# Kernel optimization log

Measured on AMD Instinct MI355X. Metric: run time of the kernel, lower is better.

Reference implementation:

```python
import jax, jax.numpy as jnp
import numpy as np

BINS = 10
LOSS_WEIGHT = 1.0
B = 8388608  # batch size
C = 2        # class num (hardcoded in the torch module's one-hot scatter)


def setup_inputs() -> dict:
    key = jax.random.key(0)
    k1, k2, k3 = jax.random.split(key, 3)
    pred = jax.random.normal(k1, (B, C), dtype=jnp.float32)
    target = jax.random.randint(k2, (B,), 0, 2, dtype=jnp.int64)
    # label_weight: 1 if valid, 0 if ignored (random 0/1 mask as float)
    label_weight = jax.random.randint(k3, (B, C), 0, 2).astype(jnp.float32)
    return {"pred": pred, "target": target, "label_weight": label_weight}


def reference(pred, target, label_weight):
    # one-hot target: torch scatter_(1, target, 1) over 2 classes
    t = jax.nn.one_hot(target, C, dtype=jnp.float32)  # [B, 2]
    # gradient norm g = |softmax(pred).detach() - target_onehot|
    g = jnp.abs(jax.lax.stop_gradient(jax.nn.softmax(pred, axis=1)) - t)  # [B, 2]
    valid = label_weight > 0
    valid_f = valid.astype(jnp.float32)
    total = jnp.maximum(valid_f.sum(), 1.0)
    # bin index: edges are i/bins with last edge nudged by 1e-6; uniform bins so
    # floor(g*bins) clipped to bins-1 reproduces the loop's (>= low) & (<= high)
    # assignment (ties on interior edges resolve to the upper bin, matching the
    # later-iteration overwrite in the torch loop).
    bin_ids = jnp.minimum((g * BINS).astype(jnp.int32), BINS - 1)  # [B, 2]
    # per-bin valid counts (histogram)
    counts = jnp.zeros((BINS,), jnp.float32).at[bin_ids].add(valid_f)
    n = jnp.maximum((counts > 0).sum().astype(jnp.float32), 1.0)
    # GHM weights: total / num_in_bin / n for valid entries, 0 otherwise
    w = jnp.where(valid, total / jnp.maximum(counts[bin_ids], 1.0) / n, 0.0)
    w = jax.lax.stop_gradient(w)
    # weighted BCE-with-logits, reduction='sum'
    bce = jnp.maximum(pred, 0.0) - pred * t + jnp.log1p(jnp.exp(-jnp.abs(pred)))
    loss = (w * bce).sum() / total
    return loss * LOSS_WEIGHT
```

## Files before the change

### kernel.cpp

```cpp
#include <hip/hip_runtime.h>

#define BINS 10
#define TPB  256
#define NBLK 2048
#define NCOPY 16

__device__ __forceinline__ unsigned long long ghm_pack(float p0, float p1, int t,
                                                       float w0, float w1, int* bin)
{
    bool tz = (t == 0);
    float x0 = tz ? -p0 : p0;
    float x1 = tz ?  p1 : -p1;
    float e0 = __expf(x0);
    float e1 = __expf(x1);
    float m  = e0 * e1;
    float g  = __fdividef(m, 1.0f + m);
    *bin = min((int)(g * 10.0f), BINS - 1);

    bool v0 = (w0 > 0.0f);
    bool v1 = (w1 > 0.0f);
    float a = v0 ? (1.0f + e0) : 1.0f;
    float b = v1 ? (1.0f + e1) : 1.0f;
    float wsum = __logf(a * b);
    unsigned long long cnt = (unsigned long long)((int)v0 + (int)v1);
    return (cnt << 48) | (unsigned long long)(unsigned int)(wsum * 1048576.0f + 0.5f);
}

__device__ __forceinline__ void ghm_2rows(float4 p, int2 t, float4 w,
                                          unsigned long long* hrow)
{
    int b0, b1;
    unsigned long long c0 = ghm_pack(p.x, p.y, t.x, w.x, w.y, &b0);
    unsigned long long c1 = ghm_pack(p.z, p.w, t.y, w.z, w.w, &b1);
    if (b0 == b1) {
        unsigned long long cs = c0 + c1;
        if (cs) atomicAdd(&hrow[b0], cs);
    } else {
        if (c0) atomicAdd(&hrow[b0], c0);
        if (c1) atomicAdd(&hrow[b1], c1);
    }
}

__global__ __launch_bounds__(TPB) void ghm_stage1(
    const float* __restrict__ pred, const int* __restrict__ target,
    const float* __restrict__ lw, unsigned long long* __restrict__ partial, int B)
{
    __shared__ unsigned long long h[NCOPY][BINS];
    for (int k = threadIdx.x; k < NCOPY * BINS; k += TPB)
        ((unsigned long long*)h)[k] = 0ULL;
    __syncthreads();

    unsigned long long* hrow = h[threadIdx.x >> 4];

    const float4* p4 = (const float4*)pred;
    const float4* w4 = (const float4*)lw;
    const int2*   t2 = (const int2*)target;
    const int npairs = B >> 1;
    const int stride = (int)gridDim.x * TPB;
    int i = blockIdx.x * TPB + threadIdx.x;

    for (; i + 3 * stride < npairs; i += 4 * stride) {
        float4 pa = p4[i];
        float4 pb = p4[i + stride];
        float4 pc = p4[i + 2 * stride];
        float4 pd = p4[i + 3 * stride];
        float4 wa = w4[i];
        float4 wb = w4[i + stride];
        float4 wc = w4[i + 2 * stride];
        float4 wd = w4[i + 3 * stride];
        int2   ta = t2[i];
        int2   tb = t2[i + stride];
        int2   tc = t2[i + 2 * stride];
        int2   td = t2[i + 3 * stride];
        ghm_2rows(pa, ta, wa, hrow);
        ghm_2rows(pb, tb, wb, hrow);
        ghm_2rows(pc, tc, wc, hrow);
        ghm_2rows(pd, td, wd, hrow);
    }
    for (; i < npairs; i += stride)
        ghm_2rows(p4[i], t2[i], w4[i], hrow);

    if ((B & 1) && blockIdx.x == 0 && threadIdx.x == 0) {
        int r = B - 1;
        int bb;
        unsigned long long cc = ghm_pack(pred[2 * r], pred[2 * r + 1], target[r],
                                         lw[2 * r], lw[2 * r + 1], &bb);
        if (cc) atomicAdd(&h[0][bb], cc);
    }
    __syncthreads();

    if (threadIdx.x < BINS) {
        unsigned long long v = 0;
#pragma unroll
        for (int c = 0; c < NCOPY; ++c) v += h[c][threadIdx.x];
        partial[blockIdx.x * BINS + threadIdx.x] = v;
    }
}

__global__ __launch_bounds__(TPB) void ghm_stage2(
    const unsigned long long* __restrict__ partial, float* __restrict__ out, int nb)
{
    double dsum[BINS], dcnt[BINS];
#pragma unroll
    for (int b = 0; b < BINS; ++b) { dsum[b] = 0.0; dcnt[b] = 0.0; }

    for (int i = threadIdx.x; i < nb; i += TPB) {
#pragma unroll
        for (int b = 0; b < BINS; ++b) {
            unsigned long long p = partial[i * BINS + b];
            dcnt[b] += (double)(p >> 48);
            dsum[b] += (double)(p & ((1ULL << 48) - 1)) * (1.0 / 1048576.0);
        }
    }

#pragma unroll
    for (int b = 0; b < BINS; ++b) {
        for (int off = 32; off > 0; off >>= 1) {
            dsum[b] += __shfl_down(dsum[b], off);
            dcnt[b] += __shfl_down(dcnt[b], off);
        }
    }

    __shared__ double ss[4][BINS];
    __shared__ double sc[4][BINS];
    const int wid  = threadIdx.x >> 6;
    const int lane = threadIdx.x & 63;
    if (lane == 0) {
#pragma unroll
        for (int b = 0; b < BINS; ++b) { ss[wid][b] = dsum[b]; sc[wid][b] = dcnt[b]; }
    }
    __syncthreads();

    if (threadIdx.x == 0) {
        double loss = 0.0;
        int n = 0;
        for (int b = 0; b < BINS; ++b) {
            double S = ss[0][b] + ss[1][b] + ss[2][b] + ss[3][b];
            double C = sc[0][b] + sc[1][b] + sc[2][b] + sc[3][b];
            if (C > 0.0) { ++n; loss += S / C; }
        }
        if (n == 0) n = 1;
        out[0] = (float)(loss / (double)n);
    }
}

extern "C" void kernel_launch(void* const* d_in, const int* in_sizes, int n_in,
                              void* d_out, int out_size, void* d_ws, size_t ws_size,
                              hipStream_t stream)
{
    const float* pred   = (const float*)d_in[0];
    const int*   target = (const int*)d_in[1];
    const float* lw     = (const float*)d_in[2];
    const int B = in_sizes[1];

    int nb = NBLK;
    size_t need = (size_t)nb * BINS * sizeof(unsigned long long);
    if (ws_size < need) nb = (int)(ws_size / (BINS * sizeof(unsigned long long)));

    unsigned long long* partial = (unsigned long long*)d_ws;

    ghm_stage1<<<nb, TPB, 0, stream>>>(pred, target, lw, partial, B);
    ghm_stage2<<<1, TPB, 0, stream>>>(partial, (float*)d_out, nb);
}
```

Baseline: 41.06 us.

## Issue all eight loads up front and transpose partials for a wider stage two

When the pair count is exactly eight grid strides, each thread issues all 24 vector loads before any computation, so more memory requests are in flight than the old four-way unrolled loop allowed. Per-block partial histograms are now stored bin-major, so stage two can read each bin with coalesced accesses across 1024 threads instead of 256. The fast path only applies when the input size matches the fixed grid exactly, and holding all loads in registers raises register pressure.

```diff
diff --git a/kernel.cpp b/kernel.cpp
--- a/kernel.cpp
+++ b/kernel.cpp
@@ -3,6 +3,7 @@
 #define BINS 10
 #define TPB  256
 #define NBLK 2048
+#define TPB2 1024
 #define NCOPY 16
 
 __device__ __forceinline__ unsigned long long ghm_pack(float p0, float p1, int t,
@@ -43,7 +44,7 @@
 
 __global__ __launch_bounds__(TPB) void ghm_stage1(
     const float* __restrict__ pred, const int* __restrict__ target,
-    const float* __restrict__ lw, unsigned long long* __restrict__ partial, int B)
+    const float* __restrict__ lw, unsigned long long* __restrict__ partialT, int B)
 {
     __shared__ unsigned long long h[NCOPY][BINS];
     for (int k = threadIdx.x; k < NCOPY * BINS; k += TPB)
@@ -57,35 +58,51 @@
     const int2*   t2 = (const int2*)target;
     const int npairs = B >> 1;
     const int stride = (int)gridDim.x * TPB;
-    int i = blockIdx.x * TPB + threadIdx.x;
+    const int i0 = blockIdx.x * TPB + threadIdx.x;
 
-    for (; i + 3 * stride < npairs; i += 4 * stride) {
-        float4 pa = p4[i];
-        float4 pb = p4[i + stride];
-        float4 pc = p4[i + 2 * stride];
-        float4 pd = p4[i + 3 * stride];
-        float4 wa = w4[i];
-        float4 wb = w4[i + stride];
-        float4 wc = w4[i + 2 * stride];
-        float4 wd = w4[i + 3 * stride];
-        int2   ta = t2[i];
-        int2   tb = t2[i + stride];
-        int2   tc = t2[i + 2 * stride];
-        int2   td = t2[i + 3 * stride];
-        ghm_2rows(pa, ta, wa, hrow);
-        ghm_2rows(pb, tb, wb, hrow);
-        ghm_2rows(pc, tc, wc, hrow);
-        ghm_2rows(pd, td, wd, hrow);
-    }
-    for (; i < npairs; i += stride)
-        ghm_2rows(p4[i], t2[i], w4[i], hrow);
-
-    if ((B & 1) && blockIdx.x == 0 && threadIdx.x == 0) {
-        int r = B - 1;
-        int bb;
-        unsigned long long cc = ghm_pack(pred[2 * r], pred[2 * r + 1], target[r],
-                                         lw[2 * r], lw[2 * r + 1], &bb);
-        if (cc) atomicAdd(&h[0][bb], cc);
+    if (npairs == 8 * stride) {
+        float4 P0 = p4[i0];
+        float4 P1 = p4[i0 + stride];
+        float4 P2 = p4[i0 + 2 * stride];
+        float4 P3 = p4[i0 + 3 * stride];
+        float4 P4 = p4[i0 + 4 * stride];
+        float4 P5 = p4[i0 + 5 * stride];
+        float4 P6 = p4[i0 + 6 * stride];
+        float4 P7 = p4[i0 + 7 * stride];
+        float4 W0 = w4[i0];
+        float4 W1 = w4[i0 + stride];
+        float4 W2 = w4[i0 + 2 * stride];
+        float4 W3 = w4[i0 + 3 * stride];
+        float4 W4 = w4[i0 + 4 * stride];
+        float4 W5 = w4[i0 + 5 * stride];
+        float4 W6 = w4[i0 + 6 * stride];
+        float4 W7 = w4[i0 + 7 * stride];
+        int2 T0 = t2[i0];
+        int2 T1 = t2[i0 + stride];
+        int2 T2 = t2[i0 + 2 * stride];
+        int2 T3 = t2[i0 + 3 * stride];
+        int2 T4 = t2[i0 + 4 * stride];
+        int2 T5 = t2[i0 + 5 * stride];
+        int2 T6 = t2[i0 + 6 * stride];
+        int2 T7 = t2[i0 + 7 * stride];
+        ghm_2rows(P0, T0, W0, hrow);
+        ghm_2rows(P1, T1, W1, hrow);
+        ghm_2rows(P2, T2, W2, hrow);
+        ghm_2rows(P3, T3, W3, hrow);
+        ghm_2rows(P4, T4, W4, hrow);
+        ghm_2rows(P5, T5, W5, hrow);
+        ghm_2rows(P6, T6, W6, hrow);
+        ghm_2rows(P7, T7, W7, hrow);
+    } else {
+        for (int i = i0; i < npairs; i += stride)
+            ghm_2rows(p4[i], t2[i], w4[i], hrow);
+        if ((B & 1) && blockIdx.x == 0 && threadIdx.x == 0) {
+            int r = B - 1;
+            int bb;
+            unsigned long long cc = ghm_pack(pred[2 * r], pred[2 * r + 1], target[r],
+                                             lw[2 * r], lw[2 * r + 1], &bb);
+            if (cc) atomicAdd(&h[0][bb], cc);
+        }
     }
     __syncthreads();
 
@@ -93,21 +110,21 @@
         unsigned long long v = 0;
 #pragma unroll
         for (int c = 0; c < NCOPY; ++c) v += h[c][threadIdx.x];
-        partial[blockIdx.x * BINS + threadIdx.x] = v;
+        partialT[threadIdx.x * gridDim.x + blockIdx.x] = v;
     }
 }
 
-__global__ __launch_bounds__(TPB) void ghm_stage2(
-    const unsigned long long* __restrict__ partial, float* __restrict__ out, int nb)
+__global__ __launch_bounds__(TPB2) void ghm_stage2(
+    const unsigned long long* __restrict__ partialT, float* __restrict__ out, int nb)
 {
     double dsum[BINS], dcnt[BINS];
 #pragma unroll
     for (int b = 0; b < BINS; ++b) { dsum[b] = 0.0; dcnt[b] = 0.0; }
 
-    for (int i = threadIdx.x; i < nb; i += TPB) {
 #pragma unroll
-        for (int b = 0; b < BINS; ++b) {
-            unsigned long long p = partial[i * BINS + b];
+    for (int b = 0; b < BINS; ++b) {
+        for (int i = threadIdx.x; i < nb; i += TPB2) {
+            unsigned long long p = partialT[b * nb + i];
             dcnt[b] += (double)(p >> 48);
             dsum[b] += (double)(p & ((1ULL << 48) - 1)) * (1.0 / 1048576.0);
         }
@@ -121,8 +138,8 @@
         }
     }
 
-    __shared__ double ss[4][BINS];
-    __shared__ double sc[4][BINS];
+    __shared__ double ss[TPB2 / 64][BINS];
+    __shared__ double sc[TPB2 / 64][BINS];
     const int wid  = threadIdx.x >> 6;
     const int lane = threadIdx.x & 63;
     if (lane == 0) {
@@ -135,8 +152,8 @@
         double loss = 0.0;
         int n = 0;
         for (int b = 0; b < BINS; ++b) {
-            double S = ss[0][b] + ss[1][b] + ss[2][b] + ss[3][b];
-            double C = sc[0][b] + sc[1][b] + sc[2][b] + sc[3][b];
+            double S = 0.0, C = 0.0;
+            for (int w = 0; w < TPB2 / 64; ++w) { S += ss[w][b]; C += sc[w][b]; }
             if (C > 0.0) { ++n; loss += S / C; }
         }
         if (n == 0) n = 1;
@@ -157,8 +174,8 @@
     size_t need = (size_t)nb * BINS * sizeof(unsigned long long);
     if (ws_size < need) nb = (int)(ws_size / (BINS * sizeof(unsigned long long)));
 
-    unsigned long long* partial = (unsigned long long*)d_ws;
+    unsigned long long* partialT = (unsigned long long*)d_ws;
 
-    ghm_stage1<<<nb, TPB, 0, stream>>>(pred, target, lw, partial, B);
-    ghm_stage2<<<1, TPB, 0, stream>>>(partial, (float*)d_out, nb);
+    ghm_stage1<<<nb, TPB, 0, stream>>>(pred, target, lw, partialT, B);
+    ghm_stage2<<<1, TPB2, 0, stream>>>(partialT, (float*)d_out, nb);
 }
```

Result: slower. 55.71 us (+35.7%).
